# Optimization experiments

Measured on AMD Instinct MI355X. Metric: run time of the kernel, lower is better.

Reference implementation:

```python
import jax, jax.numpy as jnp
import numpy as np

SWIGLU_LIMIT = 7.0
NUM_EXPERTS = 8
HIDDEN = 2880
INTER = 2880
TOKENS = 512
TOP_K = 4
W_SCALE = 0.02  # realistic init scale; keeps activations off the clamp rails


def setup_inputs() -> dict:
    key = jax.random.key(0)
    k_t, k_idx, k_gu, k_gub, k_d, k_db = jax.random.split(key, 6)
    t = jax.random.normal(k_t, (TOKENS, HIDDEN), dtype=jnp.float32)
    expert_indices = jax.random.randint(k_idx, (TOKENS, TOP_K), 0, NUM_EXPERTS)
    gate_up_proj = jax.random.normal(k_gu, (NUM_EXPERTS, 2 * INTER, HIDDEN), dtype=jnp.float32) * W_SCALE
    gate_up_proj_bias = jax.random.normal(k_gub, (NUM_EXPERTS, 2 * INTER), dtype=jnp.float32) * W_SCALE
    down_proj = jax.random.normal(k_d, (NUM_EXPERTS, HIDDEN, INTER), dtype=jnp.float32) * W_SCALE
    down_proj_bias = jax.random.normal(k_db, (NUM_EXPERTS, HIDDEN), dtype=jnp.float32) * W_SCALE
    return {
        "t": t,
        "expert_indices": expert_indices,
        "gate_up_proj": gate_up_proj,
        "gate_up_proj_bias": gate_up_proj_bias,
        "down_proj": down_proj,
        "down_proj_bias": down_proj_bias,
    }


def reference(t, expert_indices, gate_up_proj, gate_up_proj_bias, down_proj, down_proj_bias):
    # Same math as torch's gate_up_proj[expert_indices] einsum, but we avoid
    # materializing [B,K,2I,H] duplicated weights: compute all experts then gather.
    # h_all: [B, E, 2I]
    h_all = jnp.einsum('eck,bk->bec', gate_up_proj, t)
    # gather per (token, selected expert): [B, K, 2I]
    h = jnp.take_along_axis(h_all, expert_indices[:, :, None], axis=1)
    h = h + gate_up_proj_bias[expert_indices]
    x_glu = jnp.minimum(h[..., ::2], SWIGLU_LIMIT)
    x_lin = jnp.clip(h[..., 1::2], -SWIGLU_LIMIT, SWIGLU_LIMIT)
    out_glu = x_glu * jax.nn.sigmoid(1.702 * x_glu)
    u = out_glu * (x_lin + 1.0)  # [B, K, I]
    # down-proj for all experts then gather: y_all [B, K, E, H]
    y_all = jnp.einsum('ehi,bki->bkeh', down_proj, u)
    y = jnp.take_along_axis(y_all, expert_indices[:, :, None, None], axis=2)[:, :, 0, :]
    y = y + down_proj_bias[expert_indices]
    return y  # [B, K, H]
```

## Files before the change

kernel.cpp:

```cpp
#include <hip/hip_runtime.h>
#include <hip/hip_bf16.h>

#define HIDDEN   2880
#define INTER    2880
#define NEXP     8
#define GUP_ROWS 5760
#define NPAIR    2048

#define BM    320
#define PLANE_B 5120
#define KT64_B  40960
#define NKT64   45
#define KT32_B  20480
#define NKT32   90

#define MAXTILES 15
#define IMG_BYTES ((size_t)MAXTILES * NKT64 * KT64_B)

using bf16x8 = __attribute__((ext_vector_type(8))) short;
using f32x4  = __attribute__((ext_vector_type(4))) float;

typedef const __attribute__((address_space(1))) unsigned GBuf;
typedef __attribute__((address_space(3))) unsigned LBuf;

__device__ __forceinline__ void gl2lds(const void* g, void* l) {
  __builtin_amdgcn_global_load_lds((GBuf*)g, (LBuf*)l, 16, 0, 0);
}
#define WAITVM(N) { asm volatile("s_waitcnt vmcnt(" #N ")" ::: "memory"); \
                    __builtin_amdgcn_sched_barrier(0); }
__device__ __forceinline__ void barrier() {
  __builtin_amdgcn_sched_barrier(0);
  __builtin_amdgcn_s_barrier();
  __builtin_amdgcn_sched_barrier(0);
}

__device__ __forceinline__ unsigned cvt2bf(float a, float b) {
  union { __hip_bfloat16 h; unsigned short s; } x, y;
  x.h = __float2bfloat16(a);
  y.h = __float2bfloat16(b);
  return (unsigned)x.s | ((unsigned)y.s << 16);
}
__device__ __forceinline__ bf16x8 cvt8(const float4& lo, const float4& hi) {
  union { bf16x8 v; unsigned u[4]; } r;
  r.u[0] = cvt2bf(lo.x, lo.y);
  r.u[1] = cvt2bf(lo.z, lo.w);
  r.u[2] = cvt2bf(hi.x, hi.y);
  r.u[3] = cvt2bf(hi.z, hi.w);
  return r.v;
}

__global__ void route_count(const int* __restrict__ eidx, int* __restrict__ meta) {
  __shared__ int cnt[NEXP];
  int t = threadIdx.x;
  if (t < NEXP) cnt[t] = 0;
  __syncthreads();
  for (int a = t; a < NPAIR; a += 256) atomicAdd(&cnt[eidx[a]], 1);
  __syncthreads();
  if (t == 0) {
    int off = 0, toff = 0;
    for (int e = 0; e < NEXP; ++e) {
      meta[e] = cnt[e];
      meta[8 + e] = off;
      meta[16 + e] = off;
      meta[24 + e] = toff;
      off += cnt[e];
      toff += (cnt[e] + BM - 1) / BM;
    }
  }
}

__global__ void route_scatter(const int* __restrict__ eidx, int* __restrict__ meta,
                              int* __restrict__ list) {
  int a = blockIdx.x * 256 + threadIdx.x;
  int e = eidx[a];
  int pos = atomicAdd(&meta[16 + e], 1);
  list[pos] = a;
}

__global__ void gather_a(const float* __restrict__ t, const int* __restrict__ eidx,
                         const int* __restrict__ meta, const int* __restrict__ list,
                         char* __restrict__ atile) {
  const int i = blockIdx.x;
  const int a = list[i];
  const int e = eidx[a];
  const int r = i - meta[8 + e];
  const int tile = meta[24 + e] + r / BM;
  const int row = r % BM;
  const float* src = t + (size_t)(a >> 2) * HIDDEN;
  for (int ch = threadIdx.x; ch < HIDDEN / 8; ch += 256) {
    const float4* s = (const float4*)(src + ch * 8);
    float4 v0 = s[0], v1 = s[1];
    uint4 w;
    w.x = cvt2bf(v0.x, v0.y); w.y = cvt2bf(v0.z, v0.w);
    w.z = cvt2bf(v1.x, v1.y); w.w = cvt2bf(v1.z, v1.w);
    *(uint4*)(atile + ((size_t)tile * 360 + ch) * PLANE_B + row * 16) = w;
  }
}

__global__ __launch_bounds__(256, 2)
void gemm1_swiglu(const char* __restrict__ aimg,
                  const float* __restrict__ gup,
                  const float* __restrict__ gub,
                  const int* __restrict__ meta,
                  char* __restrict__ uimg)
{
  const int e = blockIdx.x, nt = blockIdx.y, mt = blockIdx.z;
  const int n_e = meta[e];
  const int m0 = mt * BM;
  if (m0 >= n_e) return;
  const int tile = meta[24 + e] + mt;
  int rows = n_e - m0; if (rows > BM) rows = BM;

  __shared__ __align__(16) char lds[2 * 32768];

  const int tid = threadIdx.x, lane = tid & 63, wid = tid >> 6;
  const int wm = wid;
  const int kq = lane >> 4, l15 = lane & 15;

  const char* aSrc = aimg + (size_t)tile * 360 * PLANE_B;
  const char* srcA[5]; int dstA[5];
  #pragma unroll
  for (int j = 0; j < 5; ++j) {
    int c = wid * 5 + j;
    srcA[j] = aSrc + c * 1024 + lane * 16;
    dstA[j] = c * 1024;
  }
  const char* srcB[3]; int dstB[3];
  #pragma unroll
  for (int j = 0; j < 3; ++j) {
    int cb = wid * 3 + j;
    int col = nt * 96 + cb * 8 + (lane >> 3);
    int g = (lane & 7) >> 1, h = lane & 1;
    srcB[j] = (const char*)gup + (size_t)(e * GUP_ROWS + col) * (HIDDEN * 4)
              + (((g ^ (col & 3)) << 5) | (h << 4));
    dstB[j] = 20480 + cb * 1024;
  }

  auto STAGE = [&](int kt, int buf) {
    char* dst = lds + buf * 32768;
    #pragma unroll
    for (int j = 0; j < 5; ++j)
      gl2lds(srcA[j] + (size_t)kt * KT32_B, dst + dstA[j]);
    #pragma unroll
    for (int j = 0; j < 3; ++j)
      gl2lds(srcB[j] + (size_t)kt * 128, dst + dstB[j]);
  };

  f32x4 acc[5][6];
  #pragma unroll
  for (int fm = 0; fm < 5; ++fm)
    #pragma unroll
    for (int fn = 0; fn < 6; ++fn)
      acc[fm][fn] = f32x4{0.f, 0.f, 0.f, 0.f};

  auto COMP = [&](int buf) {
    const char* base = lds + buf * 32768;
    const char* aB = base + kq * PLANE_B + (wm * 80 + l15) * 16;
    bf16x8 af[5], bf[6];
    #pragma unroll
    for (int fm = 0; fm < 5; ++fm) af[fm] = *(const bf16x8*)(aB + fm * 256);
    #pragma unroll
    for (int fn = 0; fn < 6; ++fn) {
      int col = fn * 16 + l15;
      const char* cp = base + 20480 + col * 128 + ((kq ^ (col & 3)) << 5);
      float4 lo = *(const float4*)cp;
      float4 hi = *(const float4*)(cp + 16);
      bf[fn] = cvt8(lo, hi);
    }
    #pragma unroll
    for (int fm = 0; fm < 5; ++fm)
      #pragma unroll
      for (int fn = 0; fn < 6; ++fn)
        acc[fm][fn] = __builtin_amdgcn_mfma_f32_16x16x32_bf16(af[fm], bf[fn], acc[fm][fn], 0, 0, 0);
  };

  STAGE(0, 0);
  for (int kt = 0; kt < NKT32; ++kt) {
    if (kt + 1 < NKT32) {
      STAGE(kt + 1, (kt + 1) & 1);
      WAITVM(8)
    } else { WAITVM(0) }
    barrier();
    COMP(kt & 1);
    barrier();
  }

  #pragma unroll
  for (int fm = 0; fm < 5; ++fm) {
    #pragma unroll
    for (int fn = 0; fn < 6; ++fn) {
      const int colg = nt * 96 + fn * 16 + l15;
      const float bias = gub[e * GUP_ROWS + colg];
      #pragma unroll
      for (int j = 0; j < 4; ++j) {
        float h = acc[fm][fn][j] + bias;
        float other = __shfl_xor(h, 1, 64);
        int rowin = wm * 80 + fm * 16 + kq * 4 + j;
        if (!(lane & 1) && rowin < rows) {
          float xg = fminf(h, 7.0f);
          float xl = fminf(fmaxf(other, -7.0f), 7.0f);
          float og = xg / (1.0f + __expf(-1.702f * xg));
          float uv = og * (xl + 1.0f);
          int uc = colg >> 1;
          *(__hip_bfloat16*)(uimg + ((size_t)tile * 360 + (uc >> 3)) * PLANE_B +
              rowin * 16 + (uc & 7) * 2) = __float2bfloat16(uv);
        }
      }
    }
  }
}

__global__ __launch_bounds__(512, 1)
void gemm2_down(const char* __restrict__ uimg,
                const float* __restrict__ dwn,
                const float* __restrict__ dbias,
                const int* __restrict__ meta,
                const int* __restrict__ list,
                float* __restrict__ out)
{
  constexpr int BN_ = 96;
  constexpr int BBUF = BN_ * 256;

  const int e = blockIdx.x, nt = blockIdx.y, mt = blockIdx.z;
  const int n_e = meta[e];
  const int m0 = mt * BM;
  if (m0 >= n_e) return;
  const int tile = meta[24 + e] + mt;
  int rows = n_e - m0; if (rows > BM) rows = BM;

  __shared__ __align__(16) char lds[2 * KT64_B + 2 * BBUF];
  char* ldsB = lds + 2 * KT64_B;

  const int tid = threadIdx.x, lane = tid & 63, wid = tid >> 6;
  const int wm = wid >> 1, wn = wid & 1;
  const int kq = lane >> 4, l15 = lane & 15;

  const char* aSrcBase = uimg + (size_t)tile * 360 * PLANE_B;
  const char* srcA[5]; int dstA[5];
  #pragma unroll
  for (int j = 0; j < 5; ++j) {
    srcA[j] = aSrcBase + wid * PLANE_B + j * 1024 + lane * 16;
    dstA[j] = wid * PLANE_B + j * 1024;
  }
  const char* srcB[3]; int dstB[3];
  #pragma unroll
  for (int j = 0; j < 3; ++j) {
    int cb = wid * 3 + j;
    int col = nt * BN_ + cb * 4 + (lane >> 4);
    int s16 = lane & 15;
    int swz = (((s16 >> 1) ^ (col & 7)) << 5) | ((s16 & 1) << 4);
    srcB[j] = (const char*)dwn + ((size_t)(e * HIDDEN + col) * INTER) * 4 + swz;
    dstB[j] = cb * 1024;
  }

  auto STAGE = [&](int kt, int buf) {
    #pragma unroll
    for (int j = 0; j < 5; ++j)
      gl2lds(srcA[j] + (size_t)kt * KT64_B, lds + buf * KT64_B + dstA[j]);
    #pragma unroll
    for (int j = 0; j < 3; ++j)
      gl2lds(srcB[j] + (size_t)kt * 256, ldsB + buf * BBUF + dstB[j]);
  };

  f32x4 acc[5][3];
  #pragma unroll
  for (int fm = 0; fm < 5; ++fm)
    #pragma unroll
    for (int fn = 0; fn < 3; ++fn)
      acc[fm][fn] = f32x4{0.f, 0.f, 0.f, 0.f};

  auto COMP = [&](int buf) {
    const char* aT = lds + buf * KT64_B;
    const char* bT = ldsB + buf * BBUF;
    #pragma unroll
    for (int s = 0; s < 2; ++s) {
      const char* aB = aT + (s * 4 + kq) * PLANE_B + (wm * 80 + l15) * 16;
      bf16x8 af[5], bf[3];
      #pragma unroll
      for (int fm = 0; fm < 5; ++fm) af[fm] = *(const bf16x8*)(aB + fm * 256);
      #pragma unroll
      for (int fn = 0; fn < 3; ++fn) {
        int col = wn * 48 + fn * 16 + l15;
        int slot = ((s * 4 + kq) ^ (col & 7)) << 5;
        const char* cp = bT + col * 256 + slot;
        float4 lo = *(const float4*)cp;
        float4 hi = *(const float4*)(cp + 16);
        bf[fn] = cvt8(lo, hi);
      }
      #pragma unroll
      for (int fm = 0; fm < 5; ++fm)
        #pragma unroll
        for (int fn = 0; fn < 3; ++fn)
          acc[fm][fn] = __builtin_amdgcn_mfma_f32_16x16x32_bf16(af[fm], bf[fn], acc[fm][fn], 0, 0, 0);
    }
  };

  STAGE(0, 0);
  for (int kt = 0; kt < NKT64; ++kt) {
    if (kt + 1 < NKT64) {
      STAGE(kt + 1, (kt + 1) & 1);
      WAITVM(8)
    } else { WAITVM(0) }
    barrier();
    COMP(kt & 1);
    barrier();
  }

  const int base = meta[8 + e];
  #pragma unroll
  for (int fm = 0; fm < 5; ++fm) {
    #pragma unroll
    for (int j = 0; j < 4; ++j) {
      int rin = wm * 80 + fm * 16 + kq * 4 + j;
      int aidx = (rin < rows) ? list[base + m0 + rin] : -1;
      #pragma unroll
      for (int fn = 0; fn < 3; ++fn) {
        int col = nt * BN_ + wn * 48 + fn * 16 + l15;
        if (aidx >= 0)
          out[(size_t)aidx * HIDDEN + col] = acc[fm][fn][j] + dbias[e * HIDDEN + col];
      }
    }
  }
}

extern "C" void kernel_launch(void* const* d_in, const int* in_sizes, int n_in,
                              void* d_out, int out_size, void* d_ws, size_t ws_size,
                              hipStream_t stream) {
  const float* t     = (const float*)d_in[0];
  const int*   eidx  = (const int*)d_in[1];
  const float* gup   = (const float*)d_in[2];
  const float* gub   = (const float*)d_in[3];
  const float* dwn   = (const float*)d_in[4];
  const float* dbias = (const float*)d_in[5];
  float* out = (float*)d_out;

  char* ws = (char*)d_ws;
  char* atile = ws;
  char* utile = ws + IMG_BYTES;
  int* meta = (int*)(ws + 2 * IMG_BYTES);
  int* list = meta + 32;

  route_count<<<1, 256, 0, stream>>>(eidx, meta);
  route_scatter<<<NPAIR / 256, 256, 0, stream>>>(eidx, meta, list);
  gather_a<<<NPAIR, 256, 0, stream>>>(t, eidx, meta, list, atile);

  dim3 g1(NEXP, GUP_ROWS / 96, 2);
  gemm1_swiglu<<<g1, 256, 0, stream>>>(atile, gup, gub, meta, utile);

  dim3 g2(NEXP, HIDDEN / 96, 2);
  gemm2_down<<<g2, 512, 0, stream>>>(utile, dwn, dbias, meta, list, out);
}
```

Before: 298.8 us.

## Retile down-projection GEMM to 64-column tiles, 4 waves, K-step 32, two blocks per CU

The down-projection kernel moves from 512-thread blocks with 96-column N tiles and 64-wide K steps to 256-thread blocks with 64-column N tiles and 32-wide K steps. Each wave now covers 80 rows by 64 columns, and the B-tile swizzle is adjusted for the smaller row stride. The aim is more blocks on the grid and two resident blocks per CU, which gives better latency hiding and load balance. In exchange it doubles the number of K iterations and barriers, and re-reads the A tile for more N tiles.

```diff
diff --git a/kernel.cpp b/kernel.cpp
--- a/kernel.cpp
+++ b/kernel.cpp
@@ -210,7 +210,7 @@
   }
 }
 
-__global__ __launch_bounds__(512, 1)
+__global__ __launch_bounds__(256, 2)
 void gemm2_down(const char* __restrict__ uimg,
                 const float* __restrict__ dwn,
                 const float* __restrict__ dbias,
@@ -218,9 +218,6 @@
                 const int* __restrict__ list,
                 float* __restrict__ out)
 {
-  constexpr int BN_ = 96;
-  constexpr int BBUF = BN_ * 256;
-
   const int e = blockIdx.x, nt = blockIdx.y, mt = blockIdx.z;
   const int n_e = meta[e];
   const int m0 = mt * BM;
@@ -228,78 +225,74 @@
   const int tile = meta[24 + e] + mt;
   int rows = n_e - m0; if (rows > BM) rows = BM;
 
-  __shared__ __align__(16) char lds[2 * KT64_B + 2 * BBUF];
-  char* ldsB = lds + 2 * KT64_B;
+  __shared__ __align__(16) char lds[2 * 20480 + 2 * 8192];
+  char* ldsB = lds + 2 * 20480;
 
   const int tid = threadIdx.x, lane = tid & 63, wid = tid >> 6;
-  const int wm = wid >> 1, wn = wid & 1;
+  const int wm = wid;
   const int kq = lane >> 4, l15 = lane & 15;
 
-  const char* aSrcBase = uimg + (size_t)tile * 360 * PLANE_B;
+  const char* aSrc = uimg + (size_t)tile * 360 * PLANE_B;
   const char* srcA[5]; int dstA[5];
   #pragma unroll
   for (int j = 0; j < 5; ++j) {
-    srcA[j] = aSrcBase + wid * PLANE_B + j * 1024 + lane * 16;
-    dstA[j] = wid * PLANE_B + j * 1024;
-  }
-  const char* srcB[3]; int dstB[3];
-  #pragma unroll
-  for (int j = 0; j < 3; ++j) {
-    int cb = wid * 3 + j;
-    int col = nt * BN_ + cb * 4 + (lane >> 4);
-    int s16 = lane & 15;
-    int swz = (((s16 >> 1) ^ (col & 7)) << 5) | ((s16 & 1) << 4);
-    srcB[j] = (const char*)dwn + ((size_t)(e * HIDDEN + col) * INTER) * 4 + swz;
+    int c = wid * 5 + j;
+    srcA[j] = aSrc + c * 1024 + lane * 16;
+    dstA[j] = c * 1024;
+  }
+  const char* srcB[2]; int dstB[2];
+  #pragma unroll
+  for (int j = 0; j < 2; ++j) {
+    int cb = wid * 2 + j;
+    int col = nt * 64 + cb * 8 + (lane >> 3);
+    int g = (lane & 7) >> 1, h = lane & 1;
+    srcB[j] = (const char*)dwn + (size_t)(e * HIDDEN + col) * (INTER * 4)
+              + (((g ^ (col & 3)) << 5) | (h << 4));
     dstB[j] = cb * 1024;
   }
 
   auto STAGE = [&](int kt, int buf) {
     #pragma unroll
     for (int j = 0; j < 5; ++j)
-      gl2lds(srcA[j] + (size_t)kt * KT64_B, lds + buf * KT64_B + dstA[j]);
-    #pragma unroll
-    for (int j = 0; j < 3; ++j)
-      gl2lds(srcB[j] + (size_t)kt * 256, ldsB + buf * BBUF + dstB[j]);
+      gl2lds(srcA[j] + (size_t)kt * KT32_B, lds + buf * 20480 + dstA[j]);
+    #pragma unroll
+    for (int j = 0; j < 2; ++j)
+      gl2lds(srcB[j] + (size_t)kt * 128, ldsB + buf * 8192 + dstB[j]);
   };
 
-  f32x4 acc[5][3];
+  f32x4 acc[5][4];
   #pragma unroll
   for (int fm = 0; fm < 5; ++fm)
     #pragma unroll
-    for (int fn = 0; fn < 3; ++fn)
+    for (int fn = 0; fn < 4; ++fn)
       acc[fm][fn] = f32x4{0.f, 0.f, 0.f, 0.f};
 
   auto COMP = [&](int buf) {
-    const char* aT = lds + buf * KT64_B;
-    const char* bT = ldsB + buf * BBUF;
-    #pragma unroll
-    for (int s = 0; s < 2; ++s) {
-      const char* aB = aT + (s * 4 + kq) * PLANE_B + (wm * 80 + l15) * 16;
-      bf16x8 af[5], bf[3];
+    const char* aB = lds + buf * 20480 + kq * PLANE_B + (wm * 80 + l15) * 16;
+    const char* bT = ldsB + buf * 8192;
+    bf16x8 af[5], bf[4];
+    #pragma unroll
+    for (int fm = 0; fm < 5; ++fm) af[fm] = *(const bf16x8*)(aB + fm * 256);
+    #pragma unroll
+    for (int fn = 0; fn < 4; ++fn) {
+      int col = fn * 16 + l15;
+      const char* cp = bT + col * 128 + ((kq ^ (col & 3)) << 5);
+      float4 lo = *(const float4*)cp;
+      float4 hi = *(const float4*)(cp + 16);
+      bf[fn] = cvt8(lo, hi);
+    }
+    #pragma unroll
+    for (int fm = 0; fm < 5; ++fm)
       #pragma unroll
-      for (int fm = 0; fm < 5; ++fm) af[fm] = *(const bf16x8*)(aB + fm * 256);
-      #pragma unroll
-      for (int fn = 0; fn < 3; ++fn) {
-        int col = wn * 48 + fn * 16 + l15;
-        int slot = ((s * 4 + kq) ^ (col & 7)) << 5;
-        const char* cp = bT + col * 256 + slot;
-        float4 lo = *(const float4*)cp;
-        float4 hi = *(const float4*)(cp + 16);
-        bf[fn] = cvt8(lo, hi);
-      }
-      #pragma unroll
-      for (int fm = 0; fm < 5; ++fm)
-        #pragma unroll
-        for (int fn = 0; fn < 3; ++fn)
-          acc[fm][fn] = __builtin_amdgcn_mfma_f32_16x16x32_bf16(af[fm], bf[fn], acc[fm][fn], 0, 0, 0);
-    }
+      for (int fn = 0; fn < 4; ++fn)
+        acc[fm][fn] = __builtin_amdgcn_mfma_f32_16x16x32_bf16(af[fm], bf[fn], acc[fm][fn], 0, 0, 0);
   };
 
   STAGE(0, 0);
-  for (int kt = 0; kt < NKT64; ++kt) {
-    if (kt + 1 < NKT64) {
+  for (int kt = 0; kt < NKT32; ++kt) {
+    if (kt + 1 < NKT32) {
       STAGE(kt + 1, (kt + 1) & 1);
-      WAITVM(8)
+      WAITVM(7)
     } else { WAITVM(0) }
     barrier();
     COMP(kt & 1);
@@ -314,8 +307,8 @@
       int rin = wm * 80 + fm * 16 + kq * 4 + j;
       int aidx = (rin < rows) ? list[base + m0 + rin] : -1;
       #pragma unroll
-      for (int fn = 0; fn < 3; ++fn) {
-        int col = nt * BN_ + wn * 48 + fn * 16 + l15;
+      for (int fn = 0; fn < 4; ++fn) {
+        int col = nt * 64 + fn * 16 + l15;
         if (aidx >= 0)
           out[(size_t)aidx * HIDDEN + col] = acc[fm][fn][j] + dbias[e * HIDDEN + col];
       }
@@ -347,6 +340,6 @@
   dim3 g1(NEXP, GUP_ROWS / 96, 2);
   gemm1_swiglu<<<g1, 256, 0, stream>>>(atile, gup, gub, meta, utile);
 
-  dim3 g2(NEXP, HIDDEN / 96, 2);
-  gemm2_down<<<g2, 512, 0, stream>>>(utile, dwn, dbias, meta, list, out);
-}
+  dim3 g2(NEXP, HIDDEN / 64, 2);
+  gemm2_down<<<g2, 256, 0, stream>>>(utile, dwn, dbias, meta, list, out);
+}
```

Result: slower. 318.5 us (+6.6%).
